# Optimization experiments

Hardware: AMD Instinct MI355X
Metric: run time of the kernel (lower is better)

The kernel has to match this reference:

```python
import jax, jax.numpy as jnp
import numpy as np

S = 16   # num_states
C = 8    # input_channels
B = 64   # batch
L = 4096 # sequence length


def hyperbolic_sigmoid(x):
    return x / (1 + jnp.abs(x)) * 0.5 + 0.5


def hyperbolic_softmax(logits, axis):
    x = hyperbolic_sigmoid(logits)
    return x / jnp.sum(x, axis=axis, keepdims=True)


def setup_inputs() -> dict:
    key = jax.random.key(0)
    k0, k1, k2, k3 = jax.random.split(key, 4)
    return {
        "log_input_probs": jax.random.normal(k0, (B, L, C), dtype=jnp.float32),
        "invh_initial_state_probs": jax.random.normal(k1, (S,), dtype=jnp.float32),
        "invh_transition_probs": jax.random.normal(k2, (S, C, S), dtype=jnp.float32),
        "invh_accepting_state_probs": jax.random.normal(k3, (S,), dtype=jnp.float32),
    }


def reference(log_input_probs, invh_initial_state_probs, invh_transition_probs, invh_accepting_state_probs):
    # hyperbolic parameterization -> probabilities
    initial_state_probs = hyperbolic_softmax(invh_initial_state_probs, axis=0)         # (S,)
    transition_probs = hyperbolic_softmax(invh_transition_probs, axis=2)               # (S,C,S)
    accepting_state_logprobs = jnp.log(hyperbolic_sigmoid(invh_accepting_state_probs)) # (S,)

    input_probs = jnp.exp(log_input_probs)  # (B,L,C)
    # per-timestep transition matrices, (B,L,S,S)
    trans_each = jnp.einsum('pcn,blc->blpn', transition_probs, input_probs)
    # log-depth chain product m0 @ m1 @ ... @ m_{L-1} via associative scan
    prefix = jax.lax.associative_scan(jnp.matmul, trans_each, axis=1)
    transition_overall = prefix[:, -1]  # (B,S,S)
    # p_state[b,n] = sum_p overall[b,p,n] * init[p]
    p_state = jnp.einsum('bpn,p->bn', transition_overall, initial_state_probs)
    log_p_state = jnp.log(p_state + 1e-20)
    log_acceptance = jax.nn.logsumexp(log_p_state + accepting_state_logprobs[None, :], axis=1)  # (B,)
    return log_acceptance[None]  # (1,B)
```

## Files before the change

### kernel.cpp

```cpp
#include <hip/hip_runtime.h>
#include <math.h>

#define S 16
#define C 8
#define NB 64
#define L 4096
#define K 64
#define LC 64

#define SLOT 324
#define RS 20

typedef __attribute__((ext_vector_type(8))) short bf16x8;
typedef __attribute__((ext_vector_type(4))) short bf16x4;
typedef __attribute__((ext_vector_type(4))) float f32x4;
typedef unsigned long long ull;

#define WS_TN   0
#define WS_INIT 8192
#define WS_ACC  8256
#define WS_CLOG 8320
#define WS_TTT  24704
#define WS_CP   57472

__device__ __forceinline__ float hsig(float x) {
    return x / (1.0f + fabsf(x)) * 0.5f + 0.5f;
}
__device__ __forceinline__ unsigned short f2bf(float f) {
    unsigned int u = __float_as_uint(f);
    return (unsigned short)((u + 0x7fffu + ((u >> 16) & 1u)) >> 16);
}

__device__ __forceinline__ bf16x8 ldfrag(const unsigned short* base, int lane) {
    int col = lane & 15, quad = lane >> 4;
    bf16x8 f = {0, 0, 0, 0, 0, 0, 0, 0};
    if (quad < 2) {
        const bf16x4* p = (const bf16x4*)(base + col * RS + quad * 8);
        bf16x4 lo = p[0], hi = p[1];
        f[0] = lo[0]; f[1] = lo[1]; f[2] = lo[2]; f[3] = lo[3];
        f[4] = hi[0]; f[5] = hi[1]; f[6] = hi[2]; f[7] = hi[3];
    }
    return f;
}

__device__ __forceinline__ f32x4 prod2(const unsigned short* slots, int sa, int sb, int lane) {
    bf16x8 a = ldfrag(slots + sa * SLOT, lane);
    bf16x8 b = ldfrag(slots + sb * SLOT, lane);
    f32x4 c = {0.f, 0.f, 0.f, 0.f};
    return __builtin_amdgcn_mfma_f32_16x16x32_bf16(a, b, c, 0, 0, 0);
}

__device__ __forceinline__ void store16(unsigned short* slot, f32x4 d, int lane, bool odd) {
    int col = lane & 15, quad = lane >> 4;
    if (odd) {
        ull pk = (ull)f2bf(d[0]) | ((ull)f2bf(d[1]) << 16)
               | ((ull)f2bf(d[2]) << 32) | ((ull)f2bf(d[3]) << 48);
        *(ull*)(slot + col * RS + quad * 4) = pk;
    } else {
#pragma unroll
        for (int r = 0; r < 4; r++) slot[(quad * 4 + r) * RS + col] = f2bf(d[r]);
    }
}

__global__ void prep_kernel(const float* __restrict__ invh_init,
                            const float* __restrict__ invh_T,
                            const float* __restrict__ invh_acc,
                            unsigned char* __restrict__ wsb) {
    int t = threadIdx.x;
    if (t < S * C) {
        float v[S]; float s = 0.f;
#pragma unroll
        for (int n = 0; n < S; n++) { v[n] = hsig(invh_T[t * S + n]); s += v[n]; }
        float inv = 1.f / s;
        float* Tn = (float*)(wsb + WS_TN);
#pragma unroll
        for (int n = 0; n < S; n++) Tn[t * S + n] = v[n] * inv;
    }
    __shared__ float si[S];
    if (t < S) si[t] = hsig(invh_init[t]);
    __syncthreads();
    if (t < S) {
        float s = 0.f;
#pragma unroll
        for (int n = 0; n < S; n++) s += si[n];
        ((float*)(wsb + WS_INIT))[t] = si[t] / s;
        ((float*)(wsb + WS_ACC))[t] = logf(hsig(invh_acc[t]));
    }
}

__global__ void prep2_kernel(unsigned char* __restrict__ wsb) {
    __shared__ float Tn[2048];
    int tid = threadIdx.x;
    const float* g = (const float*)(wsb + WS_TN);
#pragma unroll
    for (int j = 0; j < 8; j++) Tn[tid + 256 * j] = g[tid + 256 * j];
    __syncthreads();
    int cc = blockIdx.x, c = cc >> 3, cp = cc & 7;
    int p = tid >> 4, n = tid & 15;
    float acc = 0.f;
#pragma unroll
    for (int k = 0; k < S; k++) acc += Tn[p * 128 + c * 16 + k] * Tn[k * 128 + cp * 16 + n];
    ((unsigned short*)(wsb + WS_TTT))[tid * 64 + cc] = f2bf(acc);
}

__global__ void __launch_bounds__(256) chunk_kernel(const float* __restrict__ logx,
                                                    unsigned char* __restrict__ wsb) {
    __shared__ __align__(16) unsigned short slots[62 * SLOT];
    float* xs = (float*)(slots + 32 * SLOT);

    int tid = threadIdx.x, lane = tid & 63, w = tid >> 6;
    int col = lane & 15, quad = lane >> 4;
    int chunk = blockIdx.x, b = blockIdx.y;

    const unsigned short* TTT = (const unsigned short*)(wsb + WS_TTT);
    bf16x8 bfr[4][2];
#pragma unroll
    for (int jj = 0; jj < 4; jj++) {
        int t = 4 * w + jj;
#pragma unroll
        for (int kk = 0; kk < 2; kk++)
            bfr[jj][kk] = *(const bf16x8*)(TTT + (t * 16 + col) * 64 + kk * 32 + quad * 8);
    }

    const float* xg = logx + ((size_t)b * L + (size_t)chunk * LC) * C;
    xs[tid] = xg[tid];
    xs[tid + 256] = xg[tid + 256];
    __syncthreads();

    if (tid < LC) {
        float v[C]; float m = -INFINITY;
#pragma unroll
        for (int c = 0; c < C; c++) { v[c] = xs[tid * C + c]; m = fmaxf(m, v[c]); }
        float s = 0.f;
#pragma unroll
        for (int c = 0; c < C; c++) { v[c] = __expf(v[c] - m); s += v[c]; }
        float lx = m + __logf(s);
        float inv = 1.0f / s;
#pragma unroll
        for (int c = 0; c < C; c++) xs[tid * C + c] = v[c] * inv;
        float cl = lx;
#pragma unroll
        for (int d = 1; d < 64; d <<= 1) cl += __shfl_xor(cl, d);
        if (lane == 0) ((float*)(wsb + WS_CLOG))[b * K + chunk] = cl;
    }
    __syncthreads();

    bf16x8 afr[2][2];
#pragma unroll
    for (int mt = 0; mt < 2; mt++) {
        int i2 = 2 * (mt * 16 + col);
        const float4* x1p = (const float4*)(xs + (i2 + 1) * 8);
        float4 xa = x1p[0], xb = x1p[1];
#pragma unroll
        for (int kk = 0; kk < 2; kk++) {
            float x0 = xs[i2 * 8 + kk * 4 + quad];
            bf16x8 a;
            a[0] = (short)f2bf(x0 * xa.x); a[1] = (short)f2bf(x0 * xa.y);
            a[2] = (short)f2bf(x0 * xa.z); a[3] = (short)f2bf(x0 * xa.w);
            a[4] = (short)f2bf(x0 * xb.x); a[5] = (short)f2bf(x0 * xb.y);
            a[6] = (short)f2bf(x0 * xb.z); a[7] = (short)f2bf(x0 * xb.w);
            afr[mt][kk] = a;
        }
    }

#pragma unroll
    for (int mt = 0; mt < 2; mt++)
#pragma unroll
        for (int jj = 0; jj < 4; jj++) {
            f32x4 acc = {0.f, 0.f, 0.f, 0.f};
#pragma unroll
            for (int kk = 0; kk < 2; kk++)
                acc = __builtin_amdgcn_mfma_f32_16x16x32_bf16(afr[mt][kk], bfr[jj][kk], acc, 0, 0, 0);
            int t = 4 * w + jj;
#pragma unroll
            for (int r = 0; r < 4; r++) {
                int i = mt * 16 + quad * 4 + r;
                int off = (i & 1) ? (col * RS + t) : (t * RS + col);
                slots[i * SLOT + off] = f2bf(acc[r]);
            }
        }
    __syncthreads();

#pragma unroll
    for (int i2 = 0; i2 < 4; i2++) {
        int i = 4 * w + i2;
        store16(slots + (32 + i) * SLOT, prod2(slots, 2 * i, 2 * i + 1, lane), lane, i & 1);
    }
#pragma unroll
    for (int i2 = 0; i2 < 2; i2++) {
        int i = 2 * w + i2;
        store16(slots + (48 + i) * SLOT, prod2(slots, 32 + 2 * i, 32 + 2 * i + 1, lane), lane, i & 1);
    }
    store16(slots + (56 + w) * SLOT, prod2(slots, 48 + 2 * w, 48 + 2 * w + 1, lane), lane, w & 1);
    __syncthreads();
    if (w < 2)
        store16(slots + (60 + w) * SLOT, prod2(slots, 56 + 2 * w, 56 + 2 * w + 1, lane), lane, w & 1);
    __syncthreads();
    f32x4 root = prod2(slots, 60, 61, lane);

    if (w == 0) {
        unsigned short* cp = (unsigned short*)(wsb + WS_CP) + ((size_t)b * K + chunk) * 256;
        if (chunk & 1) {
            ull pk = (ull)f2bf(root[0]) | ((ull)f2bf(root[1]) << 16)
                   | ((ull)f2bf(root[2]) << 32) | ((ull)f2bf(root[3]) << 48);
            *(ull*)(cp + col * 16 + quad * 4) = pk;
        } else {
#pragma unroll
            for (int r = 0; r < 4; r++) cp[(quad * 4 + r) * 16 + col] = f2bf(root[r]);
        }
    }
}

__global__ void __launch_bounds__(256) reduce_kernel(unsigned char* __restrict__ wsb,
                                                     float* __restrict__ out) {
    __shared__ __align__(16) unsigned short slots[126 * SLOT];
    int tid = threadIdx.x, lane = tid & 63, w = tid >> 6;
    int col = lane & 15, quad = lane >> 4;
    int b = blockIdx.x;

    const uint4* src = (const uint4*)((const unsigned short*)(wsb + WS_CP) + (size_t)b * K * 256);
#pragma unroll
    for (int jj = 0; jj < 8; jj++) {
        int j = tid + 256 * jj;
        uint4 v = src[j];
        int slot = j >> 5, u = j & 31, i1 = u >> 1, half = u & 1;
        ull* d = (ull*)(slots + slot * SLOT + i1 * RS + half * 8);
        d[0] = (ull)v.x | ((ull)v.y << 32);
        d[1] = (ull)v.z | ((ull)v.w << 32);
    }
    __syncthreads();

#pragma unroll
    for (int i2 = 0; i2 < 8; i2++) {
        int i = 8 * w + i2;
        store16(slots + (64 + i) * SLOT, prod2(slots, 2 * i, 2 * i + 1, lane), lane, i & 1);
    }
#pragma unroll
    for (int i2 = 0; i2 < 4; i2++) {
        int i = 4 * w + i2;
        store16(slots + (96 + i) * SLOT, prod2(slots, 64 + 2 * i, 64 + 2 * i + 1, lane), lane, i & 1);
    }
#pragma unroll
    for (int i2 = 0; i2 < 2; i2++) {
        int i = 2 * w + i2;
        store16(slots + (112 + i) * SLOT, prod2(slots, 96 + 2 * i, 96 + 2 * i + 1, lane), lane, i & 1);
    }
    store16(slots + (120 + w) * SLOT, prod2(slots, 112 + 2 * w, 112 + 2 * w + 1, lane), lane, w & 1);
    __syncthreads();
    if (w < 2)
        store16(slots + (124 + w) * SLOT, prod2(slots, 120 + 2 * w, 120 + 2 * w + 1, lane), lane, w & 1);
    __syncthreads();
    f32x4 root = prod2(slots, 124, 125, lane);

    if (w == 0) {
        const float* initp = (const float*)(wsb + WS_INIT);
        const float* acclog = (const float*)(wsb + WS_ACC);
        float part = 0.f;
#pragma unroll
        for (int r = 0; r < 4; r++) part += initp[quad * 4 + r] * root[r];
        part += __shfl_xor(part, 16);
        part += __shfl_xor(part, 32);
        float lp = logf(part + 1e-30f) + acclog[col];
        float mx = lp;
#pragma unroll
        for (int d = 1; d < 16; d <<= 1) mx = fmaxf(mx, __shfl_xor(mx, d));
        float a2 = isfinite(mx) ? mx : 0.0f;
        float sm = expf(lp - a2);
#pragma unroll
        for (int d = 1; d < 16; d <<= 1) sm += __shfl_xor(sm, d);
        float cl = ((const float*)(wsb + WS_CLOG))[b * K + lane];
#pragma unroll
        for (int d = 1; d < 64; d <<= 1) cl += __shfl_xor(cl, d);
        if (lane == 0) out[b] = logf(sm) + a2 + cl;
    }
}

extern "C" void kernel_launch(void* const* d_in, const int* in_sizes, int n_in,
                              void* d_out, int out_size, void* d_ws, size_t ws_size,
                              hipStream_t stream) {
    const float* logx = (const float*)d_in[0];
    const float* init = (const float*)d_in[1];
    const float* T    = (const float*)d_in[2];
    const float* acc  = (const float*)d_in[3];
    unsigned char* wsb = (unsigned char*)d_ws;
    float* out = (float*)d_out;

    prep_kernel<<<1, 128, 0, stream>>>(init, T, acc, wsb);
    prep2_kernel<<<64, 256, 0, stream>>>(wsb);
    chunk_kernel<<<dim3(K, NB), 256, 0, stream>>>(logx, wsb);
    reduce_kernel<<<NB, 256, 0, stream>>>(wsb, out);
}
```

Before: 93.55 us.

## Fuse prep kernels and fold reduction into last-arriving chunk block

Merges the two parameter-prep kernels into one 256-thread block that keeps the normalized transition table in shared memory and computes the pairwise product table directly. Removes the separate reduce kernel: each chunk block bumps a per-batch atomic counter, and the last block of each batch loads all chunk products from global memory and runs the tree reduction and final logsumexp. This cuts the launch count from four to two and the gaps between them. In exchange it adds a threadfence, an atomic, and a serialized tail reduction on whichever block finishes last.

Measured after the change: 245.6 us. 163% more time.

```diff
diff --git a/kernel.cpp b/kernel.cpp
--- a/kernel.cpp
+++ b/kernel.cpp
@@ -16,12 +16,12 @@
 typedef __attribute__((ext_vector_type(4))) float f32x4;
 typedef unsigned long long ull;
 
-#define WS_TN   0
-#define WS_INIT 8192
-#define WS_ACC  8256
-#define WS_CLOG 8320
-#define WS_TTT  24704
-#define WS_CP   57472
+#define WS_INIT 0
+#define WS_ACC  64
+#define WS_CNT  128
+#define WS_CLOG 512
+#define WS_TTT  16896
+#define WS_CP   49664
 
 __device__ __forceinline__ float hsig(float x) {
     return x / (1.0f + fabsf(x)) * 0.5f + 0.5f;
@@ -50,6 +50,13 @@
     return __builtin_amdgcn_mfma_f32_16x16x32_bf16(a, b, c, 0, 0, 0);
 }
 
+__device__ __forceinline__ bf16x8 ldfrag_g(const unsigned short* base, int lane) {
+    int col = lane & 15, quad = lane >> 4;
+    bf16x8 f = {0, 0, 0, 0, 0, 0, 0, 0};
+    if (quad < 2) f = *(const bf16x8*)(base + col * 16 + quad * 8);
+    return f;
+}
+
 __device__ __forceinline__ void store16(unsigned short* slot, f32x4 d, int lane, bool odd) {
     int col = lane & 15, quad = lane >> 4;
     if (odd) {
@@ -62,22 +69,23 @@
     }
 }
 
-__global__ void prep_kernel(const float* __restrict__ invh_init,
-                            const float* __restrict__ invh_T,
-                            const float* __restrict__ invh_acc,
-                            unsigned char* __restrict__ wsb) {
+__global__ void __launch_bounds__(256) prep_kernel(const float* __restrict__ invh_init,
+                                                   const float* __restrict__ invh_T,
+                                                   const float* __restrict__ invh_acc,
+                                                   unsigned char* __restrict__ wsb) {
+    __shared__ float Tn[2048];
+    __shared__ float si[S];
     int t = threadIdx.x;
     if (t < S * C) {
         float v[S]; float s = 0.f;
 #pragma unroll
         for (int n = 0; n < S; n++) { v[n] = hsig(invh_T[t * S + n]); s += v[n]; }
         float inv = 1.f / s;
-        float* Tn = (float*)(wsb + WS_TN);
 #pragma unroll
         for (int n = 0; n < S; n++) Tn[t * S + n] = v[n] * inv;
     }
-    __shared__ float si[S];
     if (t < S) si[t] = hsig(invh_init[t]);
+    if (t < 64) ((int*)(wsb + WS_CNT))[t] = 0;
     __syncthreads();
     if (t < S) {
         float s = 0.f;
@@ -86,27 +94,29 @@
         ((float*)(wsb + WS_INIT))[t] = si[t] / s;
         ((float*)(wsb + WS_ACC))[t] = logf(hsig(invh_acc[t]));
     }
-}
-
-__global__ void prep2_kernel(unsigned char* __restrict__ wsb) {
-    __shared__ float Tn[2048];
-    int tid = threadIdx.x;
-    const float* g = (const float*)(wsb + WS_TN);
-#pragma unroll
-    for (int j = 0; j < 8; j++) Tn[tid + 256 * j] = g[tid + 256 * j];
-    __syncthreads();
-    int cc = blockIdx.x, c = cc >> 3, cp = cc & 7;
-    int p = tid >> 4, n = tid & 15;
-    float acc = 0.f;
-#pragma unroll
-    for (int k = 0; k < S; k++) acc += Tn[p * 128 + c * 16 + k] * Tn[k * 128 + cp * 16 + n];
-    ((unsigned short*)(wsb + WS_TTT))[tid * 64 + cc] = f2bf(acc);
+    int p = t >> 4, n = t & 15;
+    ull* dst = (ull*)((unsigned short*)(wsb + WS_TTT) + t * 64);
+#pragma unroll
+    for (int g = 0; g < 16; g++) {
+        ull pk = 0;
+#pragma unroll
+        for (int q = 0; q < 4; q++) {
+            int cc = 4 * g + q, c = cc >> 3, c2 = cc & 7;
+            float a = 0.f;
+#pragma unroll
+            for (int k = 0; k < S; k++) a += Tn[(p * 8 + c) * 16 + k] * Tn[(k * 8 + c2) * 16 + n];
+            pk |= (ull)f2bf(a) << (16 * q);
+        }
+        dst[g] = pk;
+    }
 }
 
 __global__ void __launch_bounds__(256) chunk_kernel(const float* __restrict__ logx,
-                                                    unsigned char* __restrict__ wsb) {
+                                                    unsigned char* __restrict__ wsb,
+                                                    float* __restrict__ out) {
     __shared__ __align__(16) unsigned short slots[62 * SLOT];
     float* xs = (float*)(slots + 32 * SLOT);
+    __shared__ int isLast;
 
     int tid = threadIdx.x, lane = tid & 63, w = tid >> 6;
     int col = lane & 15, quad = lane >> 4;
@@ -198,8 +208,9 @@
     __syncthreads();
     f32x4 root = prod2(slots, 60, 61, lane);
 
+    unsigned short* cpb = (unsigned short*)(wsb + WS_CP) + (size_t)b * K * 256;
     if (w == 0) {
-        unsigned short* cp = (unsigned short*)(wsb + WS_CP) + ((size_t)b * K + chunk) * 256;
+        unsigned short* cp = cpb + (size_t)chunk * 256;
         if (chunk & 1) {
             ull pk = (ull)f2bf(root[0]) | ((ull)f2bf(root[1]) << 16)
                    | ((ull)f2bf(root[2]) << 32) | ((ull)f2bf(root[3]) << 48);
@@ -209,58 +220,52 @@
             for (int r = 0; r < 4; r++) cp[(quad * 4 + r) * 16 + col] = f2bf(root[r]);
         }
     }
-}
-
-__global__ void __launch_bounds__(256) reduce_kernel(unsigned char* __restrict__ wsb,
-                                                     float* __restrict__ out) {
-    __shared__ __align__(16) unsigned short slots[126 * SLOT];
-    int tid = threadIdx.x, lane = tid & 63, w = tid >> 6;
-    int col = lane & 15, quad = lane >> 4;
-    int b = blockIdx.x;
-
-    const uint4* src = (const uint4*)((const unsigned short*)(wsb + WS_CP) + (size_t)b * K * 256);
-#pragma unroll
-    for (int jj = 0; jj < 8; jj++) {
-        int j = tid + 256 * jj;
-        uint4 v = src[j];
-        int slot = j >> 5, u = j & 31, i1 = u >> 1, half = u & 1;
-        ull* d = (ull*)(slots + slot * SLOT + i1 * RS + half * 8);
-        d[0] = (ull)v.x | ((ull)v.y << 32);
-        d[1] = (ull)v.z | ((ull)v.w << 32);
-    }
-    __syncthreads();
+    __syncthreads();
+
+    if (tid == 0) {
+        __threadfence();
+        int prev = atomicAdd((int*)(wsb + WS_CNT) + b, 1);
+        isLast = (prev == K - 1) ? 1 : 0;
+    }
+    __syncthreads();
+    if (!isLast) return;
+    __threadfence();
 
 #pragma unroll
     for (int i2 = 0; i2 < 8; i2++) {
         int i = 8 * w + i2;
-        store16(slots + (64 + i) * SLOT, prod2(slots, 2 * i, 2 * i + 1, lane), lane, i & 1);
+        bf16x8 a = ldfrag_g(cpb + (size_t)(2 * i) * 256, lane);
+        bf16x8 bb = ldfrag_g(cpb + (size_t)(2 * i + 1) * 256, lane);
+        f32x4 c0 = {0.f, 0.f, 0.f, 0.f};
+        f32x4 d = __builtin_amdgcn_mfma_f32_16x16x32_bf16(a, bb, c0, 0, 0, 0);
+        store16(slots + i * SLOT, d, lane, i & 1);
     }
 #pragma unroll
     for (int i2 = 0; i2 < 4; i2++) {
         int i = 4 * w + i2;
-        store16(slots + (96 + i) * SLOT, prod2(slots, 64 + 2 * i, 64 + 2 * i + 1, lane), lane, i & 1);
+        store16(slots + (32 + i) * SLOT, prod2(slots, 2 * i, 2 * i + 1, lane), lane, i & 1);
     }
 #pragma unroll
     for (int i2 = 0; i2 < 2; i2++) {
         int i = 2 * w + i2;
-        store16(slots + (112 + i) * SLOT, prod2(slots, 96 + 2 * i, 96 + 2 * i + 1, lane), lane, i & 1);
-    }
-    store16(slots + (120 + w) * SLOT, prod2(slots, 112 + 2 * w, 112 + 2 * w + 1, lane), lane, w & 1);
+        store16(slots + (48 + i) * SLOT, prod2(slots, 32 + 2 * i, 32 + 2 * i + 1, lane), lane, i & 1);
+    }
+    store16(slots + (56 + w) * SLOT, prod2(slots, 48 + 2 * w, 48 + 2 * w + 1, lane), lane, w & 1);
     __syncthreads();
     if (w < 2)
-        store16(slots + (124 + w) * SLOT, prod2(slots, 120 + 2 * w, 120 + 2 * w + 1, lane), lane, w & 1);
-    __syncthreads();
-    f32x4 root = prod2(slots, 124, 125, lane);
+        store16(slots + (60 + w) * SLOT, prod2(slots, 56 + 2 * w, 56 + 2 * w + 1, lane), lane, w & 1);
+    __syncthreads();
+    f32x4 troot = prod2(slots, 60, 61, lane);
 
     if (w == 0) {
         const float* initp = (const float*)(wsb + WS_INIT);
         const float* acclog = (const float*)(wsb + WS_ACC);
         float part = 0.f;
 #pragma unroll
-        for (int r = 0; r < 4; r++) part += initp[quad * 4 + r] * root[r];
+        for (int r = 0; r < 4; r++) part += initp[quad * 4 + r] * troot[r];
         part += __shfl_xor(part, 16);
         part += __shfl_xor(part, 32);
-        float lp = logf(part + 1e-30f) + acclog[col];
+        float lp = logf(fmaxf(part, 0.f) + 1e-30f) + acclog[col];
         float mx = lp;
 #pragma unroll
         for (int d = 1; d < 16; d <<= 1) mx = fmaxf(mx, __shfl_xor(mx, d));
@@ -285,8 +290,6 @@
     unsigned char* wsb = (unsigned char*)d_ws;
     float* out = (float*)d_out;
 
-    prep_kernel<<<1, 128, 0, stream>>>(init, T, acc, wsb);
-    prep2_kernel<<<64, 256, 0, stream>>>(wsb);
-    chunk_kernel<<<dim3(K, NB), 256, 0, stream>>>(logx, wsb);
-    reduce_kernel<<<NB, 256, 0, stream>>>(wsb, out);
-}
+    prep_kernel<<<1, 256, 0, stream>>>(init, T, acc, wsb);
+    chunk_kernel<<<dim3(K, NB), 256, 0, stream>>>(logx, wsb, out);
+}
```
